# Optimization experiments

Measured on AMD Instinct MI355X. Metric: run time of the kernel, lower is better.

Reference implementation:

```python
import jax, jax.numpy as jnp
import numpy as np

T, B, L, F, H = 32, 32, 128, 512, 1024
SCALE = 1.0 / np.sqrt(float(L))  # 1/sqrt(max_demonstration_length)


def _lstm_step(h, c, x, W_ih, W_hh, b_ih, b_hh):
    # PyTorch LSTM gate order: i, f, g, o
    gates = x @ W_ih.T + b_ih + h @ W_hh.T + b_hh
    i, f, g, o = jnp.split(gates, 4, axis=-1)
    c = jax.nn.sigmoid(f) * c + jax.nn.sigmoid(i) * jnp.tanh(g)
    h = jax.nn.sigmoid(o) * jnp.tanh(c)
    return h, c


def setup_inputs() -> dict:
    key = jax.random.key(0)
    ks = jax.random.split(key, 20)
    s = 0.02
    d = {
        'demonstration': jax.random.normal(ks[0], (T, B, L, F), jnp.float32),
        'demonstration_lengths': jax.random.randint(ks[1], (B,), 0, L),
        'current_obs': jax.random.normal(ks[2], (T, B, F), jnp.float32),
        'h0': jnp.zeros((1, B, H), jnp.float32),
        'c0': jnp.zeros((1, B, H), jnp.float32),
        # demonstration_encoder LSTM(F -> H)
        'enc_W_ih': jax.random.normal(ks[3], (4 * H, F), jnp.float32) * s,
        'enc_W_hh': jax.random.normal(ks[4], (4 * H, H), jnp.float32) * s,
        'enc_b_ih': jnp.zeros((4 * H,), jnp.float32),
        'enc_b_hh': jnp.zeros((4 * H,), jnp.float32),
        # attn Linear(H -> H)
        'attn_W': jax.random.normal(ks[5], (H, H), jnp.float32) * s,
        'attn_b': jnp.zeros((H,), jnp.float32),
        # attn_combine MLP: (F + H) -> 4H -> H
        'mlp_W1': jax.random.normal(ks[6], (4 * H, F + H), jnp.float32) * s,
        'mlp_b1': jnp.zeros((4 * H,), jnp.float32),
        'mlp_W2': jax.random.normal(ks[7], (H, 4 * H), jnp.float32) * s,
        'mlp_b2': jnp.zeros((H,), jnp.float32),
        # recurrent LSTM(H -> H)
        'lstm_W_ih': jax.random.normal(ks[8], (4 * H, H), jnp.float32) * s,
        'lstm_W_hh': jax.random.normal(ks[9], (4 * H, H), jnp.float32) * s,
        'lstm_b_ih': jnp.zeros((4 * H,), jnp.float32),
        'lstm_b_hh': jnp.zeros((4 * H,), jnp.float32),
    }
    return d


def reference(demonstration, demonstration_lengths, current_obs, h0, c0,
              enc_W_ih, enc_W_hh, enc_b_ih, enc_b_hh,
              attn_W, attn_b, mlp_W1, mlp_b1, mlp_W2, mlp_b2,
              lstm_W_ih, lstm_W_hh, lstm_b_ih, lstm_b_hh):
    # Encode demonstration[0] (B, L, F) with an LSTM over the L axis.
    x_demo = jnp.transpose(demonstration[0], (1, 0, 2))  # (L, B, F)

    def enc(carry, xt):
        h, c = carry
        h, c = _lstm_step(h, c, xt, enc_W_ih, enc_W_hh, enc_b_ih, enc_b_hh)
        return (h, c), h

    z0 = jnp.zeros((B, H), demonstration.dtype)
    _, demo_enc = jax.lax.scan(enc, (z0, z0), x_demo)  # (L, B, H)
    demo_enc = jnp.transpose(demo_enc, (1, 0, 2))       # (B, L, H)

    # attn(demo_enc) is t-invariant; hoist it out of the loop (same math).
    attn_proj = demo_enc @ attn_W.T + attn_b            # (B, L, H)

    mask = (jnp.arange(L)[None, :] < demonstration_lengths[:, None])
    mask = mask.at[:, 0].set(True)                      # (B, L)

    def step(carry, obs_t):
        h, c = carry  # (B, H)
        scores = jnp.einsum('blh,bh->bl', attn_proj, h) * SCALE
        scores = jnp.where(mask, scores, -jnp.inf)
        w = jax.nn.softmax(scores, axis=-1)             # (B, L)
        ctx = jnp.einsum('bl,blh->bh', w, demo_enc)     # (B, H)
        z = jnp.concatenate([ctx, obs_t], axis=-1)      # (B, H+F)
        m = jax.nn.relu(z @ mlp_W1.T + mlp_b1)          # MLP hidden relu
        x = jax.nn.relu(m @ mlp_W2.T + mlp_b2)          # outer relu in forward
        h, c = _lstm_step(h, c, x, lstm_W_ih, lstm_W_hh, lstm_b_ih, lstm_b_hh)
        return (h, c), h

    (hT, cT), q = jax.lax.scan(step, (h0[0], c0[0]), current_obs)
    return q, hT[None], cT[None]
```

## Files before the change

### kernel.cpp

```cpp
#include <hip/hip_runtime.h>

typedef unsigned short u16;
typedef unsigned int   u32;
typedef short s8v __attribute__((ext_vector_type(8)));
typedef short s4v __attribute__((ext_vector_type(4)));
typedef float f4v __attribute__((ext_vector_type(4)));

#define TT 32
#define BB 32
#define LL 128
#define FF 512
#define HH 1024
#define G4 4096
#define SCALE_ 0.08838834764831845f

__device__ __forceinline__ u16 f2bf(float f){
  u32 u = __float_as_uint(f);
  u32 r = u + 0x7fffu + ((u >> 16) & 1u);
  return (u16)(r >> 16);
}
__device__ __forceinline__ float bf2f(u16 s){ return __uint_as_float(((u32)s) << 16); }
__device__ __forceinline__ float sigf(float x){ return 1.f / (1.f + __expf(-x)); }

__device__ __forceinline__ void mfma16(f4v& d, s8v a, s8v b){
  asm("v_mfma_f32_16x16x32_bf16 %0, %1, %2, %0" : "+v"(d) : "v"(a), "v"(b));
}

typedef __attribute__((address_space(3))) u32 as3u32;
typedef __attribute__((address_space(1))) u32 as1u32;
__device__ __forceinline__ void glds16(const u16* g, u16* l){
  __builtin_amdgcn_global_load_lds((const as1u32*)g, (as3u32*)l, 16, 0, 0);
}

__device__ __forceinline__ void stcc_u16(u16* p, u16 v){
  u32 vv = v;
  asm volatile("global_store_short %0, %1, off sc0 sc1" :: "v"(p), "v"(vv) : "memory");
}
__device__ __forceinline__ void stcc_u32(void* p, u32 v){
  asm volatile("global_store_dword %0, %1, off sc0 sc1" :: "v"(p), "v"(v) : "memory");
}
__device__ __forceinline__ void stcc_f32(float* p, float v){
  asm volatile("global_store_dword %0, %1, off sc0 sc1" :: "v"(p), "v"(v) : "memory");
}
__device__ __forceinline__ u32 poll_ld(const u32* p){
  u32 v;
  asm volatile("global_load_dword %0, %1, off sc0 sc1\n\ts_waitcnt vmcnt(0)"
               : "=v"(v) : "v"(p) : "memory");
  return v;
}

__device__ __forceinline__ void gbar(u32* cnt, u32 nblk, u32& epoch){
  asm volatile("s_waitcnt vmcnt(0)" ::: "memory");
  __syncthreads();
  ++epoch;
  if (threadIdx.x == 0){
    atomicAdd(cnt, 1u);
    u32 target = epoch * nblk;
    while (poll_ld(cnt) < target) __builtin_amdgcn_s_sleep(1);
  }
  __syncthreads();
}

__device__ __forceinline__ void stage512_issueS(const u16* __restrict__ src, s8v* tmp, int rstride){
  const int tid = threadIdx.x;
  const int row = tid >> 4, s0 = tid & 15;
  const u16* p = src + (size_t)row * rstride + s0 * 8;
  #pragma unroll
  for (int i = 0; i < 8; i++) tmp[i] = *(const s8v*)(p + i * 128);
}
__device__ __forceinline__ void stage512_commit(const s8v* tmp, u16* lds){
  const int tid = threadIdx.x;
  const int row = tid >> 4, s0 = tid & 15;
  char* base = (char*)lds + (row << 11);
  u32 x = (u32)(row & 15) << 4;
  #pragma unroll
  for (int i = 0; i < 8; i++){
    u32 cb = (u32)(s0 + 16 * i) << 4;
    *(s8v*)(base + (cb ^ x)) = tmp[i];
  }
}
__device__ __forceinline__ s8v ldsA(const u16* lds, int row, int cb){
  return *(const s8v*)((const char*)lds + (row << 11) + (cb ^ ((row & 15) << 4)));
}

__global__ void k_convert(const float* __restrict__ src, u16* __restrict__ dst, int n){
  int i = blockIdx.x * blockDim.x + threadIdx.x;
  int st = gridDim.x * blockDim.x;
  for (; i < n; i += st) dst[i] = f2bf(src[i]);
}
__global__ void k_split_w1(const float* __restrict__ w1, u16* __restrict__ w1c, u16* __restrict__ w1o){
  int i = blockIdx.x * blockDim.x + threadIdx.x;
  int st = gridDim.x * blockDim.x;
  const int n = G4 * (FF + HH);
  for (; i < n; i += st){
    int j = i / 1536, k = i - j * 1536;
    u16 v = f2bf(w1[i]);
    if (k < HH) w1c[j * HH + k] = v;
    else        w1o[j * FF + (k - HH)] = v;
  }
}
__global__ void k_addb(const float* __restrict__ a, const float* __restrict__ b,
                       float* __restrict__ o, int n){
  int i = blockIdx.x * blockDim.x + threadIdx.x;
  int st = gridDim.x * blockDim.x;
  for (; i < n; i += st) o[i] = a[i] + b[i];
}
__global__ void k_demo_t(const float* __restrict__ d, u16* __restrict__ o){
  const int n = LL * BB * FF;
  int i = blockIdx.x * blockDim.x + threadIdx.x;
  int st = gridDim.x * blockDim.x;
  for (; i < n; i += st){
    int f = i & 511;
    int row = i >> 9;
    int l = row >> 5, b = row & 31;
    o[i] = f2bf(d[(size_t)b * (LL * FF) + l * FF + f]);
  }
}

template<int RELU>
__global__ void __launch_bounds__(256) k_gemm_bt(const u16* __restrict__ A, const u16* __restrict__ B,
        const float* __restrict__ bias, u16* __restrict__ C, int M, int N, int K)
{
  __shared__ u16 As[128 * 64];
  __shared__ u16 Bs[128 * 64];
  const int tid = threadIdx.x;
  const int lane = tid & 63, wave = tid >> 6;
  const int m0 = blockIdx.x * 128, n0 = blockIdx.y * 128;
  const int wm = wave >> 1, wn = wave & 1;
  const int lr = lane & 15, lk = (lane >> 4) * 8;
  f4v acc[4][4];
  #pragma unroll
  for (int i = 0; i < 4; i++)
    #pragma unroll
    for (int j = 0; j < 4; j++) acc[i][j] = f4v{0.f, 0.f, 0.f, 0.f};

  for (int kt = 0; kt < K; kt += 64){
    #pragma unroll
    for (int i = 0; i < 4; i++){
      int c = tid + i * 256;
      int row = c >> 3, cc = (c & 7) * 8;
      glds16(A + (size_t)(m0 + row) * K + kt + cc, &As[c * 8]);
      glds16(B + (size_t)(n0 + row) * K + kt + cc, &Bs[c * 8]);
    }
    __syncthreads();
    #pragma unroll
    for (int ks = 0; ks < 2; ++ks){
      int ko = ks * 32 + lk;
      s8v av[4], bv[4];
      #pragma unroll
      for (int m = 0; m < 4; m++) av[m] = *(const s8v*)&As[(wm * 64 + m * 16 + lr) * 64 + ko];
      #pragma unroll
      for (int n = 0; n < 4; n++) bv[n] = *(const s8v*)&Bs[(wn * 64 + n * 16 + lr) * 64 + ko];
      #pragma unroll
      for (int m = 0; m < 4; m++)
        #pragma unroll
        for (int n = 0; n < 4; n++) mfma16(acc[m][n], av[m], bv[n]);
    }
    __syncthreads();
  }
  const int r0 = (lane >> 4) * 4;
  #pragma unroll
  for (int m = 0; m < 4; m++){
    #pragma unroll
    for (int n = 0; n < 4; n++){
      int col = n0 + wn * 64 + n * 16 + lr;
      float bc = bias[col];
      #pragma unroll
      for (int r = 0; r < 4; r++){
        int row = m0 + wm * 64 + m * 16 + r0 + r;
        float v = acc[m][n][r] + bc;
        if (RELU) v = fmaxf(v, 0.f);
        C[(size_t)row * N + col] = f2bf(v);
      }
    }
  }
}

union SMemE { u16 stage[32768]; float gx[8][32][17]; };

__global__ void __launch_bounds__(512, 1) k_encoder(const u16* __restrict__ Whh, const u16* __restrict__ Xih,
      u16* __restrict__ zslot, u16* __restrict__ denc, u32* bar)
{
  __shared__ SMemE sm;
  const int nb = blockIdx.x, tid = threadIdx.x;
  const int lane = tid & 63, w = tid >> 6;
  const int jc = nb * 16;
  const int lr = lane & 15, lk = (lane >> 4) * 8;
  const int eb = tid >> 4, ejj = tid & 15;
  const int rb = (lane >> 4) * 4;

  stcc_u16(&zslot[eb * HH + jc + ejj], 0);
  float cr = 0.f;
  u32 epoch = 0;
  gbar(bar, 64, epoch);

  const int kh = (w & 1) * 512;
  const u16* Wb = Whh + (size_t)((w >> 1) * HH + jc + lr) * HH + kh + lk;
  for (int l = 0; l < LL; ++l){
    const u16* hb = (l == 0) ? zslot : (denc + (size_t)(l - 1) * (BB * HH));
    s8v ht[8];
    stage512_issueS(hb, ht, HH);
    const u16* xr = Xih + ((size_t)(l * BB + eb)) * G4 + jc + ejj;
    float xi = bf2f(xr[0]), xf = bf2f(xr[1024]), xg = bf2f(xr[2048]), xo = bf2f(xr[3072]);
    stage512_commit(ht, sm.stage);
    __syncthreads();
    f4v a0 = {0.f,0.f,0.f,0.f}, a1 = {0.f,0.f,0.f,0.f};
    #pragma unroll 8
    for (int ks = 0; ks < 16; ++ks){
      int cb = (kh + lk + ks * 32) * 2;
      s8v va0 = ldsA(sm.stage, lr,      cb);
      s8v va1 = ldsA(sm.stage, lr + 16, cb);
      s8v vb  = *(const s8v*)(Wb + ks * 32);
      mfma16(a0, va0, vb);
      mfma16(a1, va1, vb);
    }
    __syncthreads();
    #pragma unroll
    for (int r = 0; r < 4; r++){ sm.gx[w][rb + r][lr] = a0[r]; sm.gx[w][16 + rb + r][lr] = a1[r]; }
    __syncthreads();
    {
      float gi = sm.gx[0][eb][ejj] + sm.gx[1][eb][ejj] + xi;
      float gf = sm.gx[2][eb][ejj] + sm.gx[3][eb][ejj] + xf;
      float gg = sm.gx[4][eb][ejj] + sm.gx[5][eb][ejj] + xg;
      float go = sm.gx[6][eb][ejj] + sm.gx[7][eb][ejj] + xo;
      cr = sigf(gf) * cr + sigf(gi) * tanhf(gg);
      float h = sigf(go) * tanhf(cr);
      stcc_u16(&denc[(size_t)l * (BB * HH) + eb * HH + jc + ejj], f2bf(h));
    }
    gbar(bar, 64, epoch);
  }
}

union SMemD {
  u16 stage[32768];
  float gx[8][32][17];
  struct { float ssc[128]; float swt[128]; } a;
};

__global__ void __launch_bounds__(512, 1) k_decoder(
    const u16* __restrict__ aproj, const u16* __restrict__ denc, const u16* __restrict__ obsp,
    const u16* __restrict__ W1c, const u16* __restrict__ W2w, const u16* __restrict__ WihL,
    const u16* __restrict__ WhhL, const float* __restrict__ blstm, const float* __restrict__ b2,
    const float* __restrict__ h0, const float* __restrict__ c0, const int* __restrict__ lens,
    float* __restrict__ hfR, u16* __restrict__ hbR, u16* __restrict__ ctxR,
    u16* __restrict__ mbR, u16* __restrict__ xbR, float* __restrict__ out, u32* bar)
{
  __shared__ SMemD sm;
  const int nb = blockIdx.x, tid = threadIdx.x;
  const int lane = tid & 63, w = tid >> 6;
  const int jc = nb * 16;
  const int lr = lane & 15, lk = (lane >> 4) * 8;
  const int eb = tid >> 4, ejj = tid & 15;
  const int rb = (lane >> 4) * 4;

  float cr;
  {
    float hv = h0[eb * HH + jc + ejj];
    stcc_f32(&hfR[eb * HH + jc + ejj], hv);
    stcc_u16(&hbR[eb * HH + jc + ejj], f2bf(hv));
    cr = c0[eb * HH + jc + ejj];
  }
  u32 epoch = 0;
  gbar(bar, 64, epoch);

  for (int t = 0; t < TT; ++t){
    const u16* ctxS = ctxR + (size_t)t * (BB * HH);
    const u16* mbS  = mbR  + (size_t)t * (BB * G4);
    const u16* xbS  = xbR  + (size_t)t * (BB * HH);
    const u16* hbS  = hbR  + (size_t)t * (BB * HH);
    const float* hfS= hfR  + (size_t)t * (BB * HH);

    if (nb < BB){
      const int b = nb;
      const int len = lens[b];
      float hr[16];
      const float* hp = hfS + b * HH + lane * 16;
      #pragma unroll
      for (int i = 0; i < 16; i++) hr[i] = hp[i];
      for (int i = 0; i < 16; ++i){
        int l = w * 16 + i;
        const u16* ap = aproj + ((size_t)(l * BB + b)) * HH + lane * 16;
        s8v v0 = *(const s8v*)ap;
        s8v v1 = *(const s8v*)(ap + 8);
        float s = 0.f;
        #pragma unroll
        for (int k = 0; k < 8; k++) s += bf2f((u16)v0[k]) * hr[k];
        #pragma unroll
        for (int k = 0; k < 8; k++) s += bf2f((u16)v1[k]) * hr[8 + k];
        #pragma unroll
        for (int off = 32; off > 0; off >>= 1) s += __shfl_down(s, off);
        if (lane == 0){
          s *= SCALE_;
          if (l >= len && l != 0) s = -__builtin_inff();
          sm.a.ssc[l] = s;
        }
      }
      __syncthreads();
      if (w == 0){
        float x0 = sm.a.ssc[lane], x1 = sm.a.ssc[lane + 64];
        float mx = fmaxf(x0, x1);
        #pragma unroll
        for (int off = 32; off > 0; off >>= 1) mx = fmaxf(mx, __shfl_xor(mx, off));
        float e0 = __expf(x0 - mx), e1 = __expf(x1 - mx);
        float smv = e0 + e1;
        #pragma unroll
        for (int off = 32; off > 0; off >>= 1) smv += __shfl_xor(smv, off);
        float inv = 1.f / smv;
        sm.a.swt[lane] = e0 * inv;
        sm.a.swt[lane + 64] = e1 * inv;
      }
      __syncthreads();
      int hh = tid * 2;
      float a0 = 0, a1 = 0;
      #pragma unroll 4
      for (int l = 0; l < LL; ++l){
        float wv = sm.a.swt[l];
        u32 dv = *(const u32*)(denc + ((size_t)(l * BB + b)) * HH + hh);
        a0 += wv * bf2f((u16)(dv & 0xffff));
        a1 += wv * bf2f((u16)(dv >> 16));
      }
      u32 pk = ((u32)f2bf(a1) << 16) | f2bf(a0);
      stcc_u32((void*)(ctxS + b * HH + hh), pk);
    }
    gbar(bar, 64, epoch);

    {
      s8v ct[8];
      stage512_issueS(ctxS, ct, HH);
      stage512_commit(ct, sm.stage);
      __syncthreads();
      const int col0 = nb * 64 + (w >> 1) * 16;
      const int kh = (w & 1) * 512;
      f4v a0 = {0.f,0.f,0.f,0.f}, a1 = {0.f,0.f,0.f,0.f};
      const u16* Bp = W1c + (size_t)(col0 + lr) * HH + kh + lk;
      #pragma unroll 8
      for (int ks = 0; ks < 16; ++ks){
        int cb = (kh + lk + ks * 32) * 2;
        s8v va0 = ldsA(sm.stage, lr,      cb);
        s8v va1 = ldsA(sm.stage, lr + 16, cb);
        s8v vb  = *(const s8v*)(Bp + ks * 32);
        mfma16(a0, va0, vb);
        mfma16(a1, va1, vb);
      }
      __syncthreads();
      #pragma unroll
      for (int r = 0; r < 4; r++){ sm.gx[w][rb + r][lr] = a0[r]; sm.gx[w][16 + rb + r][lr] = a1[r]; }
      __syncthreads();
      #pragma unroll
      for (int cg = 0; cg < 4; ++cg){
        int col = nb * 64 + cg * 16 + ejj;
        float v = sm.gx[2 * cg][eb][ejj] + sm.gx[2 * cg + 1][eb][ejj]
                + bf2f(obsp[((size_t)(t * BB + eb)) * G4 + col]);
        stcc_u16((u16*)&mbS[eb * G4 + col], f2bf(fmaxf(v, 0.f)));
      }
    }
    gbar(bar, 64, epoch);

    {
      f4v a0 = {0.f,0.f,0.f,0.f}, a1 = {0.f,0.f,0.f,0.f};
      for (int q = 0; q < 4; ++q){
        s8v ct[8];
        stage512_issueS(mbS + q * 1024, ct, G4);
        stage512_commit(ct, sm.stage);
        __syncthreads();
        const u16* Bp = W2w + (size_t)(jc + lr) * G4 + q * 1024 + w * 128 + lk;
        #pragma unroll
        for (int ks = 0; ks < 4; ++ks){
          int cb = (w * 128 + lk + ks * 32) * 2;
          s8v va0 = ldsA(sm.stage, lr,      cb);
          s8v va1 = ldsA(sm.stage, lr + 16, cb);
          s8v vb  = *(const s8v*)(Bp + ks * 32);
          mfma16(a0, va0, vb);
          mfma16(a1, va1, vb);
        }
        __syncthreads();
      }
      #pragma unroll
      for (int r = 0; r < 4; r++){ sm.gx[w][rb + r][lr] = a0[r]; sm.gx[w][16 + rb + r][lr] = a1[r]; }
      __syncthreads();
      {
        float v = b2[jc + ejj];
        #pragma unroll
        for (int g = 0; g < 8; ++g) v += sm.gx[g][eb][ejj];
        stcc_u16((u16*)&xbS[eb * HH + jc + ejj], f2bf(fmaxf(v, 0.f)));
      }
    }
    gbar(bar, 64, epoch);

    {
      s8v xt[8], ht[8];
      stage512_issueS(xbS, xt, HH);
      stage512_issueS(hbS, ht, HH);
      stage512_commit(xt, sm.stage);
      __syncthreads();
      const int kh = (w & 1) * 512;
      f4v a0 = {0.f,0.f,0.f,0.f}, a1 = {0.f,0.f,0.f,0.f};
      const u16* Bx = WihL + (size_t)((w >> 1) * HH + jc + lr) * HH + kh + lk;
      #pragma unroll 8
      for (int ks = 0; ks < 16; ++ks){
        int cb = (kh + lk + ks * 32) * 2;
        s8v va0 = ldsA(sm.stage, lr,      cb);
        s8v va1 = ldsA(sm.stage, lr + 16, cb);
        s8v vb  = *(const s8v*)(Bx + ks * 32);
        mfma16(a0, va0, vb);
        mfma16(a1, va1, vb);
      }
      __syncthreads();
      stage512_commit(ht, sm.stage);
      __syncthreads();
      const u16* Bh = WhhL + (size_t)((w >> 1) * HH + jc + lr) * HH + kh + lk;
      #pragma unroll 8
      for (int ks = 0; ks < 16; ++ks){
        int cb = (kh + lk + ks * 32) * 2;
        s8v va0 = ldsA(sm.stage, lr,      cb);
        s8v va1 = ldsA(sm.stage, lr + 16, cb);
        s8v vb  = *(const s8v*)(Bh + ks * 32);
        mfma16(a0, va0, vb);
        mfma16(a1, va1, vb);
      }
      __syncthreads();
      #pragma unroll
      for (int r = 0; r < 4; r++){ sm.gx[w][rb + r][lr] = a0[r]; sm.gx[w][16 + rb + r][lr] = a1[r]; }
      __syncthreads();
      {
        int col = jc + ejj;
        float gi = sm.gx[0][eb][ejj] + sm.gx[1][eb][ejj] + blstm[col];
        float gf = sm.gx[2][eb][ejj] + sm.gx[3][eb][ejj] + blstm[1024 + col];
        float gg = sm.gx[4][eb][ejj] + sm.gx[5][eb][ejj] + blstm[2048 + col];
        float go = sm.gx[6][eb][ejj] + sm.gx[7][eb][ejj] + blstm[3072 + col];
        cr = sigf(gf) * cr + sigf(gi) * tanhf(gg);
        float h = sigf(go) * tanhf(cr);
        stcc_f32(&out[(size_t)t * (BB * HH) + eb * HH + col], h);
        stcc_f32(&hfR[(size_t)(t + 1) * (BB * HH) + eb * HH + col], h);
        stcc_u16(&hbR[(size_t)(t + 1) * (BB * HH) + eb * HH + col], f2bf(h));
        if (t == TT - 1){
          stcc_f32(&out[1048576 + eb * HH + col], h);
          stcc_f32(&out[1081344 + eb * HH + col], cr);
        }
      }
    }
    gbar(bar, 64, epoch);
  }
}

static constexpr size_t oWihE = 0;
static constexpr size_t oWhhE = oWihE + 4194304;
static constexpr size_t oAttnW= oWhhE + 8388608;
static constexpr size_t oW1C  = oAttnW+ 2097152;
static constexpr size_t oW1O  = oW1C  + 8388608;
static constexpr size_t oW2   = oW1O  + 4194304;
static constexpr size_t oWihL = oW2   + 8388608;
static constexpr size_t oWhhL = oWihL + 8388608;
static constexpr size_t oBEnc = oWhhL + 8388608;
static constexpr size_t oBL   = oBEnc + 16384;
static constexpr size_t oDemoT= oBL   + 16384;
static constexpr size_t oObsB = oDemoT+ 4194304;
static constexpr size_t oXih  = oObsB + 1048576;
static constexpr size_t oObsP = oXih  + 33554432;
static constexpr size_t oDEnc = oObsP + 8388608;
static constexpr size_t oAPrj = oDEnc + 8388608;
static constexpr size_t oZE   = oAPrj + 8388608;
static constexpr size_t oHFR  = oZE   + 65536;
static constexpr size_t oHBR  = oHFR  + 4325376;
static constexpr size_t oCtxR = oHBR  + 2162688;
static constexpr size_t oMBR  = oCtxR + 2097152;
static constexpr size_t oXBR  = oMBR  + 8388608;
static constexpr size_t oBar  = oXBR  + 2097152;

extern "C" void kernel_launch(void* const* d_in, const int* in_sizes, int n_in,
                              void* d_out, int out_size, void* d_ws, size_t ws_size,
                              hipStream_t stream)
{
  const float* demo = (const float*)d_in[0];
  const int*   lens = (const int*)  d_in[1];
  const float* obs  = (const float*)d_in[2];
  const float* h0   = (const float*)d_in[3];
  const float* c0   = (const float*)d_in[4];
  const float* eWih = (const float*)d_in[5];
  const float* eWhh = (const float*)d_in[6];
  const float* eBih = (const float*)d_in[7];
  const float* eBhh = (const float*)d_in[8];
  const float* aW   = (const float*)d_in[9];
  const float* aB   = (const float*)d_in[10];
  const float* W1   = (const float*)d_in[11];
  const float* B1   = (const float*)d_in[12];
  const float* W2   = (const float*)d_in[13];
  const float* B2   = (const float*)d_in[14];
  const float* lWih = (const float*)d_in[15];
  const float* lWhh = (const float*)d_in[16];
  const float* lBih = (const float*)d_in[17];
  const float* lBhh = (const float*)d_in[18];

  char* ws = (char*)d_ws;
  u16*  WihE = (u16*)(ws + oWihE);
  u16*  WhhE = (u16*)(ws + oWhhE);
  u16*  AttnW= (u16*)(ws + oAttnW);
  u16*  W1C  = (u16*)(ws + oW1C);
  u16*  W1O  = (u16*)(ws + oW1O);
  u16*  W2w  = (u16*)(ws + oW2);
  u16*  WihL = (u16*)(ws + oWihL);
  u16*  WhhL = (u16*)(ws + oWhhL);
  float* BEnc= (float*)(ws + oBEnc);
  float* BL  = (float*)(ws + oBL);
  u16*  DemoT= (u16*)(ws + oDemoT);
  u16*  ObsB = (u16*)(ws + oObsB);
  u16*  Xih  = (u16*)(ws + oXih);
  u16*  ObsP = (u16*)(ws + oObsP);
  u16*  DEnc = (u16*)(ws + oDEnc);
  u16*  APrj = (u16*)(ws + oAPrj);
  u16*  ZE   = (u16*)(ws + oZE);
  float* HFR = (float*)(ws + oHFR);
  u16*  HBR  = (u16*)(ws + oHBR);
  u16*  CtxR = (u16*)(ws + oCtxR);
  u16*  MBR  = (u16*)(ws + oMBR);
  u16*  XBR  = (u16*)(ws + oXBR);
  u32*  Bar  = (u32*)(ws + oBar);

  k_convert<<<1024, 256, 0, stream>>>(eWih, WihE, G4 * FF);
  k_convert<<<1024, 256, 0, stream>>>(eWhh, WhhE, G4 * HH);
  k_convert<<<512,  256, 0, stream>>>(aW,   AttnW, HH * HH);
  k_split_w1<<<1024, 256, 0, stream>>>(W1, W1C, W1O);
  k_convert<<<1024, 256, 0, stream>>>(W2,   W2w,  HH * G4);
  k_convert<<<1024, 256, 0, stream>>>(lWih, WihL, G4 * HH);
  k_convert<<<1024, 256, 0, stream>>>(lWhh, WhhL, G4 * HH);
  k_addb<<<16, 256, 0, stream>>>(eBih, eBhh, BEnc, G4);
  k_addb<<<16, 256, 0, stream>>>(lBih, lBhh, BL, G4);
  k_demo_t<<<1024, 256, 0, stream>>>(demo, DemoT);
  k_convert<<<512, 256, 0, stream>>>(obs, ObsB, TT * BB * FF);
  hipMemsetAsync(Bar, 0, 256, stream);

  {
    dim3 g(LL * BB / 128, G4 / 128);
    k_gemm_bt<0><<<g, 256, 0, stream>>>(DemoT, WihE, BEnc, Xih, LL * BB, G4, FF);
  }
  {
    dim3 g(TT * BB / 128, G4 / 128);
    k_gemm_bt<0><<<g, 256, 0, stream>>>(ObsB, W1O, B1, ObsP, TT * BB, G4, FF);
  }

  k_encoder<<<64, 512, 0, stream>>>(WhhE, Xih, ZE, DEnc, Bar);

  {
    dim3 g(LL * BB / 128, HH / 128);
    k_gemm_bt<0><<<g, 256, 0, stream>>>(DEnc, AttnW, aB, APrj, LL * BB, HH, HH);
  }

  k_decoder<<<64, 512, 0, stream>>>(APrj, DEnc, ObsP, W1C, W2w, WihL, WhhL,
                                    BL, B2, h0, c0, lens,
                                    HFR, HBR, CtxR, MBR, XBR, (float*)d_out, Bar + 16);
}
```

Measured before the change: 2.741 ms.

## Split decoder attention across all 64 blocks with global score exchange

```diff
diff --git a/kernel.cpp b/kernel.cpp
--- a/kernel.cpp
+++ b/kernel.cpp
@@ -234,7 +234,7 @@
 union SMemD {
   u16 stage[32768];
   float gx[8][32][17];
-  struct { float ssc[128]; float swt[128]; } a;
+  struct { float swt[128]; } a;
 };
 
 __global__ void __launch_bounds__(512, 1) k_decoder(
@@ -243,7 +243,8 @@
     const u16* __restrict__ WhhL, const float* __restrict__ blstm, const float* __restrict__ b2,
     const float* __restrict__ h0, const float* __restrict__ c0, const int* __restrict__ lens,
     float* __restrict__ hfR, u16* __restrict__ hbR, u16* __restrict__ ctxR,
-    u16* __restrict__ mbR, u16* __restrict__ xbR, float* __restrict__ out, u32* bar)
+    u16* __restrict__ mbR, u16* __restrict__ xbR, float* __restrict__ scX,
+    float* __restrict__ out, u32* bar)
 {
   __shared__ SMemD sm;
   const int nb = blockIdx.x, tid = threadIdx.x;
@@ -252,6 +253,7 @@
   const int lr = lane & 15, lk = (lane >> 4) * 8;
   const int eb = tid >> 4, ejj = tid & 15;
   const int rb = (lane >> 4) * 4;
+  const int ab = nb & 31, ah = nb >> 5;
 
   float cr;
   {
@@ -269,17 +271,17 @@
     const u16* xbS  = xbR  + (size_t)t * (BB * HH);
     const u16* hbS  = hbR  + (size_t)t * (BB * HH);
     const float* hfS= hfR  + (size_t)t * (BB * HH);
-
-    if (nb < BB){
-      const int b = nb;
-      const int len = lens[b];
+    float* scT = scX + (size_t)t * (BB * 128) + ab * 128;
+
+    {
+      const int len = lens[ab];
       float hr[16];
-      const float* hp = hfS + b * HH + lane * 16;
+      const float* hp = hfS + ab * HH + lane * 16;
       #pragma unroll
       for (int i = 0; i < 16; i++) hr[i] = hp[i];
-      for (int i = 0; i < 16; ++i){
-        int l = w * 16 + i;
-        const u16* ap = aproj + ((size_t)(l * BB + b)) * HH + lane * 16;
+      for (int i = 0; i < 8; ++i){
+        int l = ah * 64 + w * 8 + i;
+        const u16* ap = aproj + ((size_t)(l * BB + ab)) * HH + lane * 16;
         s8v v0 = *(const s8v*)ap;
         s8v v1 = *(const s8v*)(ap + 8);
         float s = 0.f;
@@ -292,12 +294,15 @@
         if (lane == 0){
           s *= SCALE_;
           if (l >= len && l != 0) s = -__builtin_inff();
-          sm.a.ssc[l] = s;
+          stcc_f32(&scT[l], s);
         }
       }
-      __syncthreads();
+    }
+    gbar(bar, 64, epoch);
+
+    {
       if (w == 0){
-        float x0 = sm.a.ssc[lane], x1 = sm.a.ssc[lane + 64];
+        float x0 = scT[lane], x1 = scT[lane + 64];
         float mx = fmaxf(x0, x1);
         #pragma unroll
         for (int off = 32; off > 0; off >>= 1) mx = fmaxf(mx, __shfl_xor(mx, off));
@@ -310,17 +315,13 @@
         sm.a.swt[lane + 64] = e1 * inv;
       }
       __syncthreads();
-      int hh = tid * 2;
-      float a0 = 0, a1 = 0;
+      int col = ah * 512 + tid;
+      const u16* dp = denc + (size_t)ab * HH + col;
+      float acc = 0.f;
       #pragma unroll 4
-      for (int l = 0; l < LL; ++l){
-        float wv = sm.a.swt[l];
-        u32 dv = *(const u32*)(denc + ((size_t)(l * BB + b)) * HH + hh);
-        a0 += wv * bf2f((u16)(dv & 0xffff));
-        a1 += wv * bf2f((u16)(dv >> 16));
-      }
-      u32 pk = ((u32)f2bf(a1) << 16) | f2bf(a0);
-      stcc_u32((void*)(ctxS + b * HH + hh), pk);
+      for (int l = 0; l < LL; ++l)
+        acc += sm.a.swt[l] * bf2f(dp[(size_t)l * (BB * HH)]);
+      stcc_u16((u16*)&ctxS[ab * HH + col], f2bf(acc));
     }
     gbar(bar, 64, epoch);
 
@@ -465,7 +466,8 @@
 static constexpr size_t oCtxR = oHBR  + 2162688;
 static constexpr size_t oMBR  = oCtxR + 2097152;
 static constexpr size_t oXBR  = oMBR  + 8388608;
-static constexpr size_t oBar  = oXBR  + 2097152;
+static constexpr size_t oScX  = oXBR  + 2097152;
+static constexpr size_t oBar  = oScX  + 524288;
 
 extern "C" void kernel_launch(void* const* d_in, const int* in_sizes, int n_in,
                               void* d_out, int out_size, void* d_ws, size_t ws_size,
@@ -514,6 +516,7 @@
   u16*  CtxR = (u16*)(ws + oCtxR);
   u16*  MBR  = (u16*)(ws + oMBR);
   u16*  XBR  = (u16*)(ws + oXBR);
+  float* ScX = (float*)(ws + oScX);
   u32*  Bar  = (u32*)(ws + oBar);
 
   k_convert<<<1024, 256, 0, stream>>>(eWih, WihE, G4 * FF);
@@ -547,5 +550,6 @@
 
   k_decoder<<<64, 512, 0, stream>>>(APrj, DEnc, ObsP, W1C, W2w, WihL, WhhL,
                                     BL, B2, h0, c0, lens,
-                                    HFR, HBR, CtxR, MBR, XBR, (float*)d_out, Bar + 16);
-}
+                                    HFR, HBR, CtxR, MBR, XBR, ScX,
+                                    (float*)d_out, Bar + 16);
+}
```

Measured after the change: 2.700 ms. About the same (-1.5%).
